# Performance work log

Hardware: AMD Instinct MI355X
Metric: run time of the kernel (lower is better)

Reference implementation:

```python
import jax, jax.numpy as jnp
import numpy as np

D_MODEL = 1024
NUM_HEADS = 16
D_K = D_MODEL // NUM_HEADS


def setup_inputs() -> dict:
    key = jax.random.key(0)
    ks = jax.random.split(key, 9)
    s = 1.0 / np.sqrt(D_MODEL)
    inp = {"x": jax.random.normal(ks[0], (4, 2048, D_MODEL), dtype=jnp.float32)}
    for i, name in enumerate(["q", "k", "v", "o"]):
        inp[f"W_{name}"] = jax.random.uniform(ks[1 + 2 * i], (D_MODEL, D_MODEL), minval=-s, maxval=s, dtype=jnp.float32)
        inp[f"b_{name}"] = jax.random.uniform(ks[2 + 2 * i], (D_MODEL,), minval=-s, maxval=s, dtype=jnp.float32)
    return inp


def reference(x, W_q, b_q, W_k, b_k, W_v, b_v, W_o, b_o):
    B, S, _ = x.shape
    # torch Linear: y = x @ W.T + b ; reshape to [B, H, S, d_k]
    def proj(W, b):
        return (x @ W.T + b).reshape(B, S, NUM_HEADS, D_K).transpose(0, 2, 1, 3)

    Q, K, V = proj(W_q, b_q), proj(W_k, b_k), proj(W_v, b_v)
    scores = jnp.einsum("bhqd,bhkd->bhqk", Q, K) / np.sqrt(D_K).astype(np.float32)
    # additive causal mask: -inf above diagonal
    causal = jnp.triu(jnp.full((S, S), -jnp.inf, dtype=scores.dtype), k=1)
    scores = scores + causal
    attn = jax.nn.softmax(scores, axis=-1)
    attn = jnp.nan_to_num(attn, nan=0.0)
    # dropout is identity in eval mode
    out = jnp.einsum("bhqk,bhkd->bhqd", attn, V)
    out = out.transpose(0, 2, 1, 3).reshape(B, S, D_MODEL)
    return out @ W_o.T + b_o
```

## Files before the change

kernel.cpp:

```cpp
#include <hip/hip_runtime.h>
#include <hip/hip_bf16.h>
#include <stdint.h>

#define D_MODEL 1024
#define SEQ     2048
#define NH      16
#define DK      64
#define PSTR    72

typedef __bf16 bf16x8 __attribute__((ext_vector_type(8)));
typedef float  f32x4  __attribute__((ext_vector_type(4)));
typedef unsigned short u16;

__device__ __forceinline__ u16 f2bf(float f) {
    uint32_t u = __float_as_uint(f);
    u += 0x7FFFu + ((u >> 16) & 1u);
    return (u16)(u >> 16);
}

__device__ __forceinline__ void gl2lds16(const u16* g, u16* l) {
    __builtin_amdgcn_global_load_lds(
        (const __attribute__((address_space(1))) uint32_t*)g,
        (__attribute__((address_space(3))) uint32_t*)l, 16, 0, 0);
}

__global__ __launch_bounds__(256) void cvt_kernel(const float* __restrict__ src,
                                                  u16* __restrict__ dst, int n4) {
    int i = blockIdx.x * blockDim.x + threadIdx.x;
    if (i >= n4) return;
    float4 v = reinterpret_cast<const float4*>(src)[i];
    ushort4 o;
    o.x = f2bf(v.x); o.y = f2bf(v.y); o.z = f2bf(v.z); o.w = f2bf(v.w);
    reinterpret_cast<ushort4*>(dst)[i] = o;
}

__global__ __launch_bounds__(256) void cvt4_kernel(
    const float* __restrict__ s0, const float* __restrict__ s1,
    const float* __restrict__ s2, const float* __restrict__ s3,
    u16* __restrict__ d0, u16* __restrict__ d1,
    u16* __restrict__ d2, u16* __restrict__ d3, int n4) {
    int z = blockIdx.y;
    const float* s = (z == 0) ? s0 : (z == 1) ? s1 : (z == 2) ? s2 : s3;
    u16* d = (z == 0) ? d0 : (z == 1) ? d1 : (z == 2) ? d2 : d3;
    int i = blockIdx.x * blockDim.x + threadIdx.x;
    if (i >= n4) return;
    float4 v = reinterpret_cast<const float4*>(s)[i];
    ushort4 o;
    o.x = f2bf(v.x); o.y = f2bf(v.y); o.z = f2bf(v.z); o.w = f2bf(v.w);
    reinterpret_cast<ushort4*>(d)[i] = o;
}

__device__ __forceinline__ void gemm128_body(const u16* __restrict__ Ag,
                                             const u16* __restrict__ Bg,
                                             u16* As, u16* Bs, f32x4 acc[4][4]) {
    const int K = D_MODEL;
    int tid = threadIdx.x, wave = tid >> 6, lane = tid & 63;
    int l15 = lane & 15, quad = lane >> 4;
    int srow = lane >> 2;
    int scol = (lane & 3) * 8;
    int arg4 = (wave >> 1) * 4;
    int brg4 = (wave & 1) * 4;
#pragma unroll 1
    for (int kc = 0; kc < K; kc += 64) {
        __syncthreads();
#pragma unroll
        for (int j = 0; j < 4; ++j) {
            int p = wave * 4 + j;
            int rg = p >> 1, h = p & 1;
            int row = rg * 16 + srow;
            int col = kc + h * 32 + scol;
            gl2lds16(Ag + row * K + col, As + p * 512);
            gl2lds16(Bg + row * K + col, Bs + p * 512);
        }
        __syncthreads();
#pragma unroll
        for (int h = 0; h < 2; ++h) {
            bf16x8 af[4], bfr[4];
#pragma unroll
            for (int s = 0; s < 4; ++s) {
                af[s]  = *reinterpret_cast<const bf16x8*>(
                    As + ((arg4 + s) * 2 + h) * 512 + l15 * 32 + quad * 8);
                bfr[s] = *reinterpret_cast<const bf16x8*>(
                    Bs + ((brg4 + s) * 2 + h) * 512 + l15 * 32 + quad * 8);
            }
#pragma unroll
            for (int ms = 0; ms < 4; ++ms)
#pragma unroll
                for (int ns = 0; ns < 4; ++ns)
                    acc[ms][ns] = __builtin_amdgcn_mfma_f32_16x16x32_bf16(
                        af[ms], bfr[ns], acc[ms][ns], 0, 0, 0);
        }
    }
}

__global__ __launch_bounds__(256) void qkv_gemm(
    const u16* __restrict__ xb,
    const u16* __restrict__ Wq, const u16* __restrict__ Wk, const u16* __restrict__ Wv,
    const float* __restrict__ bq, const float* __restrict__ bk, const float* __restrict__ bv,
    u16* __restrict__ qo, u16* __restrict__ ko, u16* __restrict__ vto) {
    __shared__ __align__(16) u16 As[16 * 512], Bs[16 * 512];
    int z = blockIdx.z;
    const u16* W = (z == 0) ? Wq : (z == 1) ? Wk : Wv;
    const float* bias = (z == 0) ? bq : (z == 1) ? bk : bv;
    int lane = threadIdx.x & 63, wave = threadIdx.x >> 6;
    int l15 = lane & 15, quad = lane >> 4;
    int mw = blockIdx.x * 128 + (wave >> 1) * 64;
    int nw = blockIdx.y * 128 + (wave & 1) * 64;

    f32x4 acc[4][4];
#pragma unroll
    for (int ms = 0; ms < 4; ++ms)
#pragma unroll
        for (int ns = 0; ns < 4; ++ns)
            acc[ms][ns] = (f32x4){0.f, 0.f, 0.f, 0.f};

    gemm128_body(xb + blockIdx.x * 128 * D_MODEL, W + blockIdx.y * 128 * D_MODEL,
                 As, Bs, acc);

    const float qscale = 0.125f * 1.4426950408889634f;
#pragma unroll
    for (int ns = 0; ns < 4; ++ns) {
        int n = nw + ns * 16 + l15;
        float bv_ = bias[n];
        int h = n >> 6, d = n & 63;
#pragma unroll
        for (int ms = 0; ms < 4; ++ms) {
            int mbase = mw + ms * 16 + quad * 4;
            int b = mbase >> 11, s = mbase & (SEQ - 1);
            int bh = b * NH + h;
            if (z == 2) {
                ushort4 pk;
                pk.x = f2bf(acc[ms][ns][0] + bv_);
                pk.y = f2bf(acc[ms][ns][1] + bv_);
                pk.z = f2bf(acc[ms][ns][2] + bv_);
                pk.w = f2bf(acc[ms][ns][3] + bv_);
                *reinterpret_cast<ushort4*>(&vto[(bh * DK + d) * SEQ + s]) = pk;
            } else {
                u16* dst = (z == 0) ? qo : ko;
                float sc = (z == 0) ? qscale : 1.0f;
#pragma unroll
                for (int r = 0; r < 4; ++r)
                    dst[(bh * SEQ + s + r) * DK + d] = f2bf((acc[ms][ns][r] + bv_) * sc);
            }
        }
    }
}

__global__ __launch_bounds__(256) void out_gemm(
    const u16* __restrict__ ab, const u16* __restrict__ Wo,
    const float* __restrict__ bo, float* __restrict__ out) {
    __shared__ __align__(16) u16 As[16 * 512], Bs[16 * 512];
    int lane = threadIdx.x & 63, wave = threadIdx.x >> 6;
    int l15 = lane & 15, quad = lane >> 4;
    int mw = blockIdx.x * 128 + (wave >> 1) * 64;
    int nw = blockIdx.y * 128 + (wave & 1) * 64;

    f32x4 acc[4][4];
#pragma unroll
    for (int ms = 0; ms < 4; ++ms)
#pragma unroll
        for (int ns = 0; ns < 4; ++ns)
            acc[ms][ns] = (f32x4){0.f, 0.f, 0.f, 0.f};

    gemm128_body(ab + blockIdx.x * 128 * D_MODEL, Wo + blockIdx.y * 128 * D_MODEL,
                 As, Bs, acc);

#pragma unroll
    for (int ns = 0; ns < 4; ++ns) {
        int n = nw + ns * 16 + l15;
        float bv_ = bo[n];
#pragma unroll
        for (int ms = 0; ms < 4; ++ms) {
            int mbase = mw + ms * 16 + quad * 4;
#pragma unroll
            for (int r = 0; r < 4; ++r)
                out[(mbase + r) * D_MODEL + n] = acc[ms][ns][r] + bv_;
        }
    }
}

__global__ __launch_bounds__(256, 2) void attn_kernel(
    const u16* __restrict__ Q, const u16* __restrict__ Kc,
    const u16* __restrict__ Vt, u16* __restrict__ ao) {
    __shared__ __align__(16) u16 Ks[8 * 512], Vs[8 * 512], Plds[4][32 * PSTR];
    int pair = blockIdx.x, bh = blockIdx.y;
    int lane = threadIdx.x & 63, wave = threadIdx.x >> 6;
    int l15 = lane & 15, quad = lane >> 4;
    const u16* Qb = Q + bh * (SEQ * DK);
    const u16* Kb = Kc + bh * (SEQ * DK);
    const u16* Vb = Vt + bh * (DK * SEQ);
    int b = bh >> 4, hh = bh & 15;
    u16* Pw = &Plds[wave][0];

#pragma unroll 1
    for (int ti = 0; ti < 2; ++ti) {
        int t = ti ? (15 - pair) : pair;
        int q0w = t * 128 + wave * 32;
        int qmax = q0w + 31;

        bf16x8 qf[2][2];
#pragma unroll
        for (int nf = 0; nf < 2; ++nf)
#pragma unroll
            for (int h = 0; h < 2; ++h)
                qf[nf][h] = *reinterpret_cast<const bf16x8*>(
                    Qb + (q0w + nf * 16 + l15) * DK + h * 32 + quad * 8);

        f32x4 o[2][4];
#pragma unroll
        for (int ma = 0; ma < 2; ++ma)
#pragma unroll
            for (int nf = 0; nf < 4; ++nf)
                o[ma][nf] = (f32x4){0.f, 0.f, 0.f, 0.f};
        float lsum[2] = {0.f, 0.f};

        int nch = 2 * t + 2;
#pragma unroll 1
        for (int c = 0; c < nch; ++c) {
            int k0 = c * 64;
            __syncthreads();
#pragma unroll
            for (int h = 0; h < 2; ++h) {
                gl2lds16(Kb + (k0 + wave * 16 + l15) * DK + h * 32 + quad * 8,
                         Ks + (wave * 2 + h) * 512);
                gl2lds16(Vb + (wave * 16 + l15) * SEQ + k0 + h * 32 + quad * 8,
                         Vs + (wave * 2 + h) * 512);
            }
            __syncthreads();
            if (k0 > qmax) continue;

            f32x4 s[4][2];
#pragma unroll
            for (int mf = 0; mf < 4; ++mf) {
                bf16x8 kf0 = *reinterpret_cast<const bf16x8*>(Ks + (mf * 2 + 0) * 512 + lane * 8);
                bf16x8 kf1 = *reinterpret_cast<const bf16x8*>(Ks + (mf * 2 + 1) * 512 + lane * 8);
#pragma unroll
                for (int nf = 0; nf < 2; ++nf) {
                    f32x4 z = (f32x4){0.f, 0.f, 0.f, 0.f};
                    z = __builtin_amdgcn_mfma_f32_16x16x32_bf16(kf0, qf[nf][0], z, 0, 0, 0);
                    z = __builtin_amdgcn_mfma_f32_16x16x32_bf16(kf1, qf[nf][1], z, 0, 0, 0);
                    s[mf][nf] = z;
                }
            }
            if (k0 + 63 > q0w) {
#pragma unroll
                for (int mf = 0; mf < 4; ++mf) {
                    int key = k0 + mf * 16 + quad * 4;
#pragma unroll
                    for (int nf = 0; nf < 2; ++nf) {
                        int q = q0w + nf * 16 + l15;
#pragma unroll
                        for (int r = 0; r < 4; ++r)
                            if (key + r > q) s[mf][nf][r] = -__builtin_inff();
                    }
                }
            }
#pragma unroll
            for (int mf = 0; mf < 4; ++mf)
#pragma unroll
                for (int nf = 0; nf < 2; ++nf) {
                    float p0 = __builtin_amdgcn_exp2f(s[mf][nf][0]);
                    float p1 = __builtin_amdgcn_exp2f(s[mf][nf][1]);
                    float p2 = __builtin_amdgcn_exp2f(s[mf][nf][2]);
                    float p3 = __builtin_amdgcn_exp2f(s[mf][nf][3]);
                    lsum[nf] += (p0 + p1) + (p2 + p3);
                    ushort4 pk;
                    pk.x = f2bf(p0); pk.y = f2bf(p1); pk.z = f2bf(p2); pk.w = f2bf(p3);
                    *reinterpret_cast<ushort4*>(
                        Pw + (nf * 16 + l15) * PSTR + mf * 16 + quad * 4) = pk;
                }
            __asm__ volatile("s_waitcnt lgkmcnt(0)" ::: "memory");
            bf16x8 pa[2][2];
#pragma unroll
            for (int ma = 0; ma < 2; ++ma)
#pragma unroll
                for (int h = 0; h < 2; ++h)
                    pa[ma][h] = *reinterpret_cast<const bf16x8*>(
                        Pw + (ma * 16 + l15) * PSTR + h * 32 + quad * 8);
#pragma unroll
            for (int nf = 0; nf < 4; ++nf) {
                bf16x8 vf0 = *reinterpret_cast<const bf16x8*>(Vs + (nf * 2 + 0) * 512 + lane * 8);
                bf16x8 vf1 = *reinterpret_cast<const bf16x8*>(Vs + (nf * 2 + 1) * 512 + lane * 8);
#pragma unroll
                for (int ma = 0; ma < 2; ++ma) {
                    o[ma][nf] = __builtin_amdgcn_mfma_f32_16x16x32_bf16(pa[ma][0], vf0, o[ma][nf], 0, 0, 0);
                    o[ma][nf] = __builtin_amdgcn_mfma_f32_16x16x32_bf16(pa[ma][1], vf1, o[ma][nf], 0, 0, 0);
                }
            }
        }
        lsum[0] += __shfl_xor(lsum[0], 16);
        lsum[0] += __shfl_xor(lsum[0], 32);
        lsum[1] += __shfl_xor(lsum[1], 16);
        lsum[1] += __shfl_xor(lsum[1], 32);
#pragma unroll
        for (int ma = 0; ma < 2; ++ma) {
#pragma unroll
            for (int r = 0; r < 4; ++r) {
                float inv = __builtin_amdgcn_rcpf(__shfl(lsum[ma], quad * 4 + r));
                int q = q0w + ma * 16 + quad * 4 + r;
#pragma unroll
                for (int nf = 0; nf < 4; ++nf) {
                    int d = nf * 16 + l15;
                    ao[(b * SEQ + q) * D_MODEL + hh * DK + d] = f2bf(o[ma][nf][r] * inv);
                }
            }
        }
    }
}

extern "C" void kernel_launch(void* const* d_in, const int* in_sizes, int n_in,
                              void* d_out, int out_size, void* d_ws, size_t ws_size,
                              hipStream_t stream) {
    const float* x  = (const float*)d_in[0];
    const float* Wq = (const float*)d_in[1];
    const float* bq = (const float*)d_in[2];
    const float* Wk = (const float*)d_in[3];
    const float* bk = (const float*)d_in[4];
    const float* Wv = (const float*)d_in[5];
    const float* bv = (const float*)d_in[6];
    const float* Wo = (const float*)d_in[7];
    const float* bo = (const float*)d_in[8];
    float* out = (float*)d_out;
    char* ws = (char*)d_ws;

    const size_t XB = 16777216;
    const size_t WB = 2097152;
    u16* xb  = (u16*)(ws);
    u16* wqb = (u16*)(ws + XB);
    u16* wkb = (u16*)(ws + XB + WB);
    u16* wvb = (u16*)(ws + XB + 2 * WB);
    u16* wob = (u16*)(ws + XB + 3 * WB);
    u16* qb  = (u16*)(ws + XB + 4 * WB);
    u16* kb  = (u16*)(ws + 2 * XB + 4 * WB);
    u16* vtb = (u16*)(ws + 3 * XB + 4 * WB);
    u16* ab  = (u16*)(ws + 4 * XB + 4 * WB);

    cvt_kernel<<<8192, 256, 0, stream>>>(x, xb, 2097152);
    cvt4_kernel<<<dim3(1024, 4), 256, 0, stream>>>(Wq, Wk, Wv, Wo,
                                                   wqb, wkb, wvb, wob, 262144);

    qkv_gemm<<<dim3(64, 8, 3), 256, 0, stream>>>(xb, wqb, wkb, wvb, bq, bk, bv,
                                                 qb, kb, vtb);
    attn_kernel<<<dim3(8, 64), 256, 0, stream>>>(qb, kb, vtb, ab);
    out_gemm<<<dim3(64, 8), 256, 0, stream>>>(ab, wob, bo, out);
}
```

Before: 269.1 us.

## Rewrite QKV projection GEMM as 256x256 tiled, double-buffered 8-wave pipeline

Replaces the 128x128 QKV GEMM with a 256x256 tile kernel using 512 threads (8 waves), each wave computing a 128x64 subtile. Global-to-LDS loads go into double-buffered, XOR-swizzled shared memory and are staged in quarters that interleave with MFMA phases, with barriers and s_setprio around the math. The intent is more data reuse per loaded byte, fewer LDS bank conflicts, and overlap of loads with compute. In exchange it uses more registers and LDS, launches far fewer blocks (384), and relies on fragile manual waitcnt and barrier scheduling.

```diff
diff --git a/kernel.cpp b/kernel.cpp
--- a/kernel.cpp
+++ b/kernel.cpp
@@ -11,6 +11,8 @@
 typedef __bf16 bf16x8 __attribute__((ext_vector_type(8)));
 typedef float  f32x4  __attribute__((ext_vector_type(4)));
 typedef unsigned short u16;
+
+#define CFENCE() asm volatile("" ::: "memory")
 
 __device__ __forceinline__ u16 f2bf(float f) {
     uint32_t u = __float_as_uint(f);
@@ -93,54 +95,181 @@
     }
 }
 
-__global__ __launch_bounds__(256) void qkv_gemm(
+__device__ __forceinline__ void stage_half(const u16* __restrict__ gb, u16* ls,
+                                           int w2, int srow, int scol) {
+#pragma unroll
+    for (int i = 0; i < 2; ++i)
+        gl2lds16(gb + ((w2 + i) * 8 + srow) * D_MODEL + scol,
+                 ls + (w2 + i) * 512);
+}
+
+__global__ __launch_bounds__(512, 2) void qkv_gemm256(
     const u16* __restrict__ xb,
     const u16* __restrict__ Wq, const u16* __restrict__ Wk, const u16* __restrict__ Wv,
     const float* __restrict__ bq, const float* __restrict__ bk, const float* __restrict__ bv,
     u16* __restrict__ qo, u16* __restrict__ ko, u16* __restrict__ vto) {
-    __shared__ __align__(16) u16 As[16 * 512], Bs[16 * 512];
+    __shared__ __align__(16) u16 smA[2][2][8192];
+    __shared__ __align__(16) u16 smB[2][2][8192];
     int z = blockIdx.z;
     const u16* W = (z == 0) ? Wq : (z == 1) ? Wk : Wv;
     const float* bias = (z == 0) ? bq : (z == 1) ? bk : bv;
-    int lane = threadIdx.x & 63, wave = threadIdx.x >> 6;
+    int tid = threadIdx.x;
+    int lane = tid & 63, wave = tid >> 6;
     int l15 = lane & 15, quad = lane >> 4;
-    int mw = blockIdx.x * 128 + (wave >> 1) * 64;
-    int nw = blockIdx.y * 128 + (wave & 1) * 64;
-
-    f32x4 acc[4][4];
-#pragma unroll
-    for (int ms = 0; ms < 4; ++ms)
-#pragma unroll
-        for (int ns = 0; ns < 4; ++ns)
-            acc[ms][ns] = (f32x4){0.f, 0.f, 0.f, 0.f};
-
-    gemm128_body(xb + blockIdx.x * 128 * D_MODEL, W + blockIdx.y * 128 * D_MODEL,
-                 As, Bs, acc);
-
+    int wr = wave >> 2, wc = wave & 3;
+    int w2 = wave * 2;
+    const u16* Abase = xb + (size_t)blockIdx.x * 256 * D_MODEL;
+    const u16* Bbase = W + (size_t)blockIdx.y * 256 * D_MODEL;
+
+    int u = (lane * 16) ^ ((lane >> 5) << 5);
+    int srow = u >> 7;
+    int scol = (u & 127) >> 1;
+    int sx = ((l15 >> 2) & 1) << 5;
+    int c0 = ((quad * 16) ^ sx) >> 1;
+    int c1 = ((64 + quad * 16) ^ sx) >> 1;
+    int rb0 = (wc & 1) * 64;
+
+    f32x4 acc[8][4];
+#pragma unroll
+    for (int m = 0; m < 8; ++m)
+#pragma unroll
+        for (int n = 0; n < 4; ++n) acc[m][n] = (f32x4){0.f, 0.f, 0.f, 0.f};
+
+    stage_half(Abase, &smA[0][0][0], w2, srow, scol);
+    stage_half(Abase + 128 * D_MODEL, &smA[0][1][0], w2, srow, scol);
+    stage_half(Bbase, &smB[0][0][0], w2, srow, scol);
+    stage_half(Bbase + 128 * D_MODEL, &smB[0][1][0], w2, srow, scol);
+    stage_half(Abase + 64, &smA[1][0][0], w2, srow, scol);
+    asm volatile("s_waitcnt vmcnt(2)" ::: "memory");
+    __builtin_amdgcn_s_barrier();
+    CFENCE();
+
+#pragma unroll 1
+    for (int t = 0; t < 16; ++t) {
+        const int p = t & 1;
+        const u16* As = &smA[p][wr][0];
+        const u16* Bs = &smB[p][wc >> 1][0];
+        bf16x8 af[4][2], bfr[2][2];
+
+#pragma unroll
+        for (int m = 0; m < 4; ++m) {
+            af[m][0] = *reinterpret_cast<const bf16x8*>(As + (m * 16 + l15) * 64 + c0);
+            af[m][1] = *reinterpret_cast<const bf16x8*>(As + (m * 16 + l15) * 64 + c1);
+        }
+#pragma unroll
+        for (int nn = 0; nn < 2; ++nn) {
+            bfr[nn][0] = *reinterpret_cast<const bf16x8*>(Bs + (rb0 + nn * 16 + l15) * 64 + c0);
+            bfr[nn][1] = *reinterpret_cast<const bf16x8*>(Bs + (rb0 + nn * 16 + l15) * 64 + c1);
+        }
+        if (t < 15) stage_half(Abase + 128 * D_MODEL + (t + 1) * 64,
+                               &smA[(t + 1) & 1][1][0], w2, srow, scol);
+        CFENCE(); __builtin_amdgcn_s_barrier(); CFENCE();
+        __builtin_amdgcn_s_setprio(1);
+#pragma unroll
+        for (int m = 0; m < 4; ++m)
+#pragma unroll
+            for (int nn = 0; nn < 2; ++nn) {
+                acc[m][nn] = __builtin_amdgcn_mfma_f32_16x16x32_bf16(af[m][0], bfr[nn][0], acc[m][nn], 0, 0, 0);
+                acc[m][nn] = __builtin_amdgcn_mfma_f32_16x16x32_bf16(af[m][1], bfr[nn][1], acc[m][nn], 0, 0, 0);
+            }
+        __builtin_amdgcn_s_setprio(0);
+        CFENCE(); __builtin_amdgcn_s_barrier(); CFENCE();
+
+#pragma unroll
+        for (int nn = 0; nn < 2; ++nn) {
+            bfr[nn][0] = *reinterpret_cast<const bf16x8*>(Bs + (rb0 + (2 + nn) * 16 + l15) * 64 + c0);
+            bfr[nn][1] = *reinterpret_cast<const bf16x8*>(Bs + (rb0 + (2 + nn) * 16 + l15) * 64 + c1);
+        }
+        if (t < 15) stage_half(Bbase + (t + 1) * 64,
+                               &smB[(t + 1) & 1][0][0], w2, srow, scol);
+        CFENCE(); __builtin_amdgcn_s_barrier(); CFENCE();
+        __builtin_amdgcn_s_setprio(1);
+#pragma unroll
+        for (int m = 0; m < 4; ++m)
+#pragma unroll
+            for (int nn = 0; nn < 2; ++nn) {
+                acc[m][2 + nn] = __builtin_amdgcn_mfma_f32_16x16x32_bf16(af[m][0], bfr[nn][0], acc[m][2 + nn], 0, 0, 0);
+                acc[m][2 + nn] = __builtin_amdgcn_mfma_f32_16x16x32_bf16(af[m][1], bfr[nn][1], acc[m][2 + nn], 0, 0, 0);
+            }
+        __builtin_amdgcn_s_setprio(0);
+        CFENCE(); __builtin_amdgcn_s_barrier(); CFENCE();
+
+#pragma unroll
+        for (int m = 0; m < 4; ++m) {
+            af[m][0] = *reinterpret_cast<const bf16x8*>(As + ((m + 4) * 16 + l15) * 64 + c0);
+            af[m][1] = *reinterpret_cast<const bf16x8*>(As + ((m + 4) * 16 + l15) * 64 + c1);
+        }
+#pragma unroll
+        for (int nn = 0; nn < 2; ++nn) {
+            bfr[nn][0] = *reinterpret_cast<const bf16x8*>(Bs + (rb0 + nn * 16 + l15) * 64 + c0);
+            bfr[nn][1] = *reinterpret_cast<const bf16x8*>(Bs + (rb0 + nn * 16 + l15) * 64 + c1);
+        }
+        if (t < 15) stage_half(Bbase + 128 * D_MODEL + (t + 1) * 64,
+                               &smB[(t + 1) & 1][1][0], w2, srow, scol);
+        CFENCE(); __builtin_amdgcn_s_barrier(); CFENCE();
+        __builtin_amdgcn_s_setprio(1);
+#pragma unroll
+        for (int m = 0; m < 4; ++m)
+#pragma unroll
+            for (int nn = 0; nn < 2; ++nn) {
+                acc[4 + m][nn] = __builtin_amdgcn_mfma_f32_16x16x32_bf16(af[m][0], bfr[nn][0], acc[4 + m][nn], 0, 0, 0);
+                acc[4 + m][nn] = __builtin_amdgcn_mfma_f32_16x16x32_bf16(af[m][1], bfr[nn][1], acc[4 + m][nn], 0, 0, 0);
+            }
+        __builtin_amdgcn_s_setprio(0);
+        CFENCE(); __builtin_amdgcn_s_barrier(); CFENCE();
+
+#pragma unroll
+        for (int nn = 0; nn < 2; ++nn) {
+            bfr[nn][0] = *reinterpret_cast<const bf16x8*>(Bs + (rb0 + (2 + nn) * 16 + l15) * 64 + c0);
+            bfr[nn][1] = *reinterpret_cast<const bf16x8*>(Bs + (rb0 + (2 + nn) * 16 + l15) * 64 + c1);
+        }
+        if (t < 14) stage_half(Abase + (t + 2) * 64,
+                               &smA[p][0][0], w2, srow, scol);
+        CFENCE(); __builtin_amdgcn_s_barrier(); CFENCE();
+        __builtin_amdgcn_s_setprio(1);
+#pragma unroll
+        for (int m = 0; m < 4; ++m)
+#pragma unroll
+            for (int nn = 0; nn < 2; ++nn) {
+                acc[4 + m][2 + nn] = __builtin_amdgcn_mfma_f32_16x16x32_bf16(af[m][0], bfr[nn][0], acc[4 + m][2 + nn], 0, 0, 0);
+                acc[4 + m][2 + nn] = __builtin_amdgcn_mfma_f32_16x16x32_bf16(af[m][1], bfr[nn][1], acc[4 + m][2 + nn], 0, 0, 0);
+            }
+        __builtin_amdgcn_s_setprio(0);
+        if (t < 14) {
+            asm volatile("s_waitcnt vmcnt(2)" ::: "memory");
+            __builtin_amdgcn_s_barrier(); CFENCE();
+        } else if (t == 14) {
+            asm volatile("s_waitcnt vmcnt(0)" ::: "memory");
+            __builtin_amdgcn_s_barrier(); CFENCE();
+        }
+    }
+
+    int mw = blockIdx.x * 256 + wr * 128;
+    int nwb = blockIdx.y * 256 + wc * 64;
     const float qscale = 0.125f * 1.4426950408889634f;
 #pragma unroll
-    for (int ns = 0; ns < 4; ++ns) {
-        int n = nw + ns * 16 + l15;
+    for (int nf = 0; nf < 4; ++nf) {
+        int n = nwb + nf * 16 + l15;
         float bv_ = bias[n];
         int h = n >> 6, d = n & 63;
 #pragma unroll
-        for (int ms = 0; ms < 4; ++ms) {
-            int mbase = mw + ms * 16 + quad * 4;
+        for (int mf = 0; mf < 8; ++mf) {
+            int mbase = mw + mf * 16 + quad * 4;
             int b = mbase >> 11, s = mbase & (SEQ - 1);
             int bh = b * NH + h;
             if (z == 2) {
                 ushort4 pk;
-                pk.x = f2bf(acc[ms][ns][0] + bv_);
-                pk.y = f2bf(acc[ms][ns][1] + bv_);
-                pk.z = f2bf(acc[ms][ns][2] + bv_);
-                pk.w = f2bf(acc[ms][ns][3] + bv_);
+                pk.x = f2bf(acc[mf][nf][0] + bv_);
+                pk.y = f2bf(acc[mf][nf][1] + bv_);
+                pk.z = f2bf(acc[mf][nf][2] + bv_);
+                pk.w = f2bf(acc[mf][nf][3] + bv_);
                 *reinterpret_cast<ushort4*>(&vto[(bh * DK + d) * SEQ + s]) = pk;
             } else {
                 u16* dst = (z == 0) ? qo : ko;
                 float sc = (z == 0) ? qscale : 1.0f;
 #pragma unroll
                 for (int r = 0; r < 4; ++r)
-                    dst[(bh * SEQ + s + r) * DK + d] = f2bf((acc[ms][ns][r] + bv_) * sc);
+                    dst[(bh * SEQ + s + r) * DK + d] = f2bf((acc[mf][nf][r] + bv_) * sc);
             }
         }
     }
@@ -339,8 +468,8 @@
     cvt4_kernel<<<dim3(1024, 4), 256, 0, stream>>>(Wq, Wk, Wv, Wo,
                                                    wqb, wkb, wvb, wob, 262144);
 
-    qkv_gemm<<<dim3(64, 8, 3), 256, 0, stream>>>(xb, wqb, wkb, wvb, bq, bk, bv,
-                                                 qb, kb, vtb);
+    qkv_gemm256<<<dim3(32, 4, 3), 512, 0, stream>>>(xb, wqb, wkb, wvb, bq, bk, bv,
+                                                    qb, kb, vtb);
     attn_kernel<<<dim3(8, 64), 256, 0, stream>>>(qb, kb, vtb, ab);
     out_gemm<<<dim3(64, 8), 256, 0, stream>>>(ab, wob, bo, out);
 }
```

Measured after the change: 288.5 us. 7.2% more time.
